# Kernel optimization log

Measured on AMD Instinct MI355X. Metric: run time of the kernel, lower is better.

## Reference

```python
import jax, jax.numpy as jnp
import numpy as np

B, T, C = 2, 2048, 1024
E = 8            # num_experts
K = 2            # num_active (top-k)
H = 4 * C        # expert hidden dim


def setup_inputs() -> dict:
    key = jax.random.key(0)
    ks = jax.random.split(key, 8)
    s = 0.02
    return {
        "x": jax.random.normal(ks[0], (B, T, C), dtype=jnp.float32),
        "Wg": jax.random.normal(ks[1], (C, E), dtype=jnp.float32) * s,
        "bg": jnp.zeros((E,), dtype=jnp.float32),
        "W1": jax.random.normal(ks[2], (E, C, H), dtype=jnp.float32) * s,
        "b1": jnp.zeros((E, H), dtype=jnp.float32),
        "W2": jax.random.normal(ks[3], (E, H, C), dtype=jnp.float32) * s,
        "b2": jnp.zeros((E, C), dtype=jnp.float32),
    }


def reference(x, Wg, bg, W1, b1, W2, b2):
    Bs, Ts, Cs = x.shape
    x_flat = x.reshape(-1, Cs)                       # [N, C]
    gate_logits = x_flat @ Wg + bg                   # [N, E]
    gates = jax.nn.softmax(gate_logits, axis=-1)
    w, idx = jax.lax.top_k(gates, K)                 # [N, K]
    w = w / jnp.sum(w, axis=-1, keepdims=True)
    # combine[n, e] = sum_k w[n,k] * (idx[n,k] == e); zero for unrouted experts,
    # so weighting the dense per-expert output reproduces the masked scatter-add.
    combine = jnp.sum(jax.nn.one_hot(idx, E, dtype=x.dtype) * w[..., None], axis=1)  # [N, E]
    out = jnp.zeros_like(x_flat)
    for e in range(E):  # small fixed expert loop; GEMM-dominated
        h = jax.nn.gelu(x_flat @ W1[e] + b1[e], approximate=False)  # [N, H]
        y = h @ W2[e] + b2[e]                                       # [N, C]
        out = out + y * combine[:, e:e + 1]
    return out.reshape(Bs, Ts, Cs)
```

## Files before the change

kernel.cpp:

```cpp
#include <hip/hip_runtime.h>
#include <hip/hip_bf16.h>
#include <math.h>

#define NTOK  4096
#define CDIM  1024
#define HDIM  4096
#define NEXP  8
#define TOPK  2

using short8 = __attribute__((ext_vector_type(8))) short;
using f32x4  = __attribute__((ext_vector_type(4))) float;

__device__ inline ushort f2bf(float f) {
    uint32_t u = __builtin_bit_cast(uint32_t, f);
    uint32_t r = (u + 0x7FFFu + ((u >> 16) & 1u)) >> 16;
    return (ushort)r;
}

__device__ __forceinline__ void gl_lds16(const void* g, void* l) {
    __builtin_amdgcn_global_load_lds(
        (const __attribute__((address_space(1))) void*)(void*)g,
        (__attribute__((address_space(3))) void*)l, 16, 0, 0);
}

__global__ __launch_bounds__(256)
void gate_kernel(const float* __restrict__ x, const float* __restrict__ Wg,
                 const float* __restrict__ bg, int* __restrict__ counts,
                 int* __restrict__ tlist, float* __restrict__ wslot,
                 ushort* __restrict__ xbf) {
    int wave = threadIdx.x >> 6, lane = threadIdx.x & 63;
    int t = blockIdx.x * 4 + wave;
    const float* xr = x + (size_t)t * CDIM;

    float acc[NEXP];
#pragma unroll
    for (int e = 0; e < NEXP; e++) acc[e] = 0.f;

#pragma unroll
    for (int i = 0; i < CDIM / 64; i++) {
        int c = lane + 64 * i;
        float xv = xr[c];
        xbf[(size_t)t * CDIM + c] = f2bf(xv);
        const float* wr = Wg + (size_t)c * NEXP;
#pragma unroll
        for (int e = 0; e < NEXP; e++) acc[e] += xv * wr[e];
    }
#pragma unroll
    for (int e = 0; e < NEXP; e++) {
        float v = acc[e];
        for (int off = 32; off > 0; off >>= 1) v += __shfl_xor(v, off);
        acc[e] = v + bg[e];
    }
    if (lane == 0) {
        int i1 = 0; float m1 = acc[0];
#pragma unroll
        for (int e = 1; e < NEXP; e++) if (acc[e] > m1) { m1 = acc[e]; i1 = e; }
        int i2 = -1; float m2 = -1e30f;
#pragma unroll
        for (int e = 0; e < NEXP; e++) if (e != i1 && acc[e] > m2) { m2 = acc[e]; i2 = e; }
        float w0 = 1.f / (1.f + expf(m2 - m1));
        float w1 = 1.f - w0;
        int p0 = atomicAdd(&counts[i1], 1);
        tlist[i1 * NTOK + p0] = t * 2;
        int p1 = atomicAdd(&counts[i2], 1);
        tlist[i2 * NTOK + p1] = t * 2 + 1;
        wslot[t * 2]     = w0;
        wslot[t * 2 + 1] = w1;
    }
}

__global__ __launch_bounds__(256)
void transpose_kernel(const float* __restrict__ in, ushort* __restrict__ out,
                      int R, int Ccols) {
    __shared__ ushort tile[64 * 64];
    int e = blockIdx.z;
    const float* src = in + (size_t)e * R * Ccols;
    ushort* dst = out + (size_t)e * Ccols * R;
    int c0 = blockIdx.x * 64, r0 = blockIdx.y * 64;
    int tid = threadIdx.x;
    int tx = tid & 15, ty = tid >> 4;

    float4 v[4];
#pragma unroll
    for (int j = 0; j < 4; j++)
        v[j] = *(const float4*)&src[(size_t)(r0 + ty * 4 + j) * Ccols + c0 + tx * 4];

#pragma unroll
    for (int i = 0; i < 4; i++) {
        int c = tx * 4 + i;
        uint2 pr;
        pr.x = (uint)f2bf(v[0][i]) | ((uint)f2bf(v[1][i]) << 16);
        pr.y = (uint)f2bf(v[2][i]) | ((uint)f2bf(v[3][i]) << 16);
        int gr = (ty >> 1) ^ ((c >> 2) & 7);
        int off = c * 128 + (gr << 4) + (ty & 1) * 8;
        *(uint2*)((char*)tile + off) = pr;
    }
    __syncthreads();

#pragma unroll
    for (int p = 0; p < 2; p++) {
        int c   = (tid >> 3) + 32 * p;
        int rch = tid & 7;
        int gr  = rch ^ ((c >> 2) & 7);
        short8 val = *(short8*)((char*)tile + c * 128 + (gr << 4));
        *(short8*)&dst[(size_t)(c0 + c) * R + r0 + rch * 8] = val;
    }
}

template<int GELU, int OUTBF16>
__global__ __launch_bounds__(256, 3)
void moe_gemm(const ushort* __restrict__ A, const ushort* __restrict__ Bt,
              const float* __restrict__ bias, const int* __restrict__ tlist,
              const int* __restrict__ counts, void* __restrict__ Out,
              int K, int N, int ashift, int nxmask, int nxshift, int ksplit,
              size_t psz) {
    int flat = blockIdx.x;
    int e  = flat & 7;
    int j  = flat >> 3;
    int mt = j & 31;
    int nj = j >> 5;
    int cnt = counts[e];
    int m0 = mt * 128;
    if (m0 >= cnt) return;
    int n0 = (nj & nxmask) * 128;
    int split = nj >> nxshift;
    int kbeg = split * ksplit;

    __shared__ ushort As[2][128 * 32];
    __shared__ ushort Bs[2][128 * 32];
    __shared__ int rowv[128];

    int tid = threadIdx.x;
    if (tid < 128) {
        int r = m0 + tid;
        rowv[tid] = tlist[e * NTOK + (r < cnt ? r : cnt - 1)];
    }
    __syncthreads();

    const ushort* Be = Bt + (size_t)e * N * K;

    int lane = tid & 63, w = tid >> 6;
    int wm = (w >> 1) * 64, wn = (w & 1) * 64;
    int quad = lane >> 4, l16 = lane & 15;

    int srow   = tid >> 2;
    int schunk = (tid & 3) ^ ((tid >> 3) & 3);
    const ushort* pa0 = A  + (size_t)(rowv[srow]      >> ashift) * K + kbeg + schunk * 8;
    const ushort* pa1 = A  + (size_t)(rowv[srow + 64] >> ashift) * K + kbeg + schunk * 8;
    const ushort* pb0 = Be + (size_t)(n0 + srow)      * K + kbeg + schunk * 8;
    const ushort* pb1 = Be + (size_t)(n0 + srow + 64) * K + kbeg + schunk * 8;

    int swr  = quad ^ ((l16 >> 1) & 3);
    int aidx = (wm + l16) * 32 + swr * 8;
    int bidx = (wn + l16) * 32 + swr * 8;

    f32x4 acc[4][4] = {};

    auto STAGE = [&](int buf) {
        gl_lds16(pa0, &As[buf][(w * 16) * 32]);
        gl_lds16(pa1, &As[buf][(w * 16 + 64) * 32]);
        gl_lds16(pb0, &Bs[buf][(w * 16) * 32]);
        gl_lds16(pb1, &Bs[buf][(w * 16 + 64) * 32]);
        pa0 += 32; pa1 += 32; pb0 += 32; pb1 += 32;
    };
    auto COMPUTE = [&](int buf) {
        short8 a[4], b[4];
#pragma unroll
        for (int mti = 0; mti < 4; mti++) a[mti] = *(short8*)&As[buf][aidx + mti * 512];
#pragma unroll
        for (int nti = 0; nti < 4; nti++) b[nti] = *(short8*)&Bs[buf][bidx + nti * 512];
#pragma unroll
        for (int mti = 0; mti < 4; mti++)
#pragma unroll
            for (int nti = 0; nti < 4; nti++)
                acc[mti][nti] = __builtin_amdgcn_mfma_f32_16x16x32_bf16(
                    a[mti], b[nti], acc[mti][nti], 0, 0, 0);
    };

    int nsteps = ksplit >> 5;
    STAGE(0);
    __syncthreads();
    for (int i = 0; i < nsteps - 2; i += 2) {
        STAGE(1);
        COMPUTE(0);
        __syncthreads();
        STAGE(0);
        COMPUTE(1);
        __syncthreads();
    }
    STAGE(1);
    COMPUTE(0);
    __syncthreads();
    COMPUTE(1);

    float* outF = (float*)Out + split * psz;
    ushort* outH = (ushort*)Out;
    const float* be = bias + (size_t)e * N;
#pragma unroll
    for (int mti = 0; mti < 4; mti++) {
#pragma unroll
        for (int r = 0; r < 4; r++) {
            int lrow = wm + mti * 16 + quad * 4 + r;
            if (m0 + lrow < cnt) {
                int v = rowv[lrow];
                size_t base = (size_t)v * N;
#pragma unroll
                for (int nti = 0; nti < 4; nti++) {
                    int col = n0 + wn + nti * 16 + l16;
                    float val = acc[mti][nti][r] + (split == 0 ? be[col] : 0.f);
                    if (GELU) val = 0.5f * val * (1.0f + erff(val * 0.70710678118654752f));
                    if (OUTBF16) outH[base + col] = f2bf(val);
                    else         outF[base + col] = val;
                }
            }
        }
    }
}

__global__ __launch_bounds__(256)
void combine_kernel(const float* __restrict__ y, const float* __restrict__ wslot,
                    float* __restrict__ out) {
    const float* y2 = y + (size_t)NTOK * TOPK * CDIM;
    int idx = blockIdx.x * 256 + threadIdx.x;
    int c4 = idx & (CDIM / 4 - 1);
    int t = idx >> 8;
    float w0 = wslot[2 * t], w1 = wslot[2 * t + 1];
    const float4* y0a = (const float4*)(y  + (size_t)(2 * t) * CDIM);
    const float4* y1a = (const float4*)(y  + (size_t)(2 * t + 1) * CDIM);
    const float4* y0b = (const float4*)(y2 + (size_t)(2 * t) * CDIM);
    const float4* y1b = (const float4*)(y2 + (size_t)(2 * t + 1) * CDIM);
    float4 a0 = y0a[c4], a1 = y0b[c4], b0 = y1a[c4], b1 = y1b[c4], o;
    o.x = w0 * (a0.x + a1.x) + w1 * (b0.x + b1.x);
    o.y = w0 * (a0.y + a1.y) + w1 * (b0.y + b1.y);
    o.z = w0 * (a0.z + a1.z) + w1 * (b0.z + b1.z);
    o.w = w0 * (a0.w + a1.w) + w1 * (b0.w + b1.w);
    ((float4*)(out + (size_t)t * CDIM))[c4] = o;
}

extern "C" void kernel_launch(void* const* d_in, const int* in_sizes, int n_in,
                              void* d_out, int out_size, void* d_ws, size_t ws_size,
                              hipStream_t stream) {
    const float* x  = (const float*)d_in[0];
    const float* Wg = (const float*)d_in[1];
    const float* bg = (const float*)d_in[2];
    const float* W1 = (const float*)d_in[3];
    const float* b1 = (const float*)d_in[4];
    const float* W2 = (const float*)d_in[5];
    const float* b2 = (const float*)d_in[6];
    float* out = (float*)d_out;
    char* ws = (char*)d_ws;

    size_t off = 0;
    int*    counts = (int*)(ws + off);    off += 256;
    int*    tlist  = (int*)(ws + off);    off += (size_t)NEXP * NTOK * 4;
    float*  wslot  = (float*)(ws + off);  off += (size_t)NTOK * TOPK * 4;
    ushort* xbf    = (ushort*)(ws + off); off += (size_t)NTOK * CDIM * 2;
    ushort* WT     = (ushort*)(ws + off); off += (size_t)NEXP * CDIM * HDIM * 2;
    ushort* h      = (ushort*)(ws + off); off += (size_t)NTOK * TOPK * HDIM * 2;
    float*  y      = (float*)(ws + off);  off += (size_t)NTOK * TOPK * CDIM * 4 * 2;

    hipMemsetAsync(counts, 0, NEXP * sizeof(int), stream);

    gate_kernel<<<NTOK / 4, 256, 0, stream>>>(x, Wg, bg, counts, tlist, wslot, xbf);

    transpose_kernel<<<dim3(HDIM / 64, CDIM / 64, NEXP), 256, 0, stream>>>(
        W1, WT, CDIM, HDIM);

    moe_gemm<1, 1><<<NEXP * 32 * (HDIM / 128), 256, 0, stream>>>(
        xbf, WT, b1, tlist, counts, (void*)h, CDIM, HDIM, 1,
        HDIM / 128 - 1, 5, CDIM, 0);

    transpose_kernel<<<dim3(CDIM / 64, HDIM / 64, NEXP), 256, 0, stream>>>(
        W2, WT, HDIM, CDIM);

    moe_gemm<0, 0><<<NEXP * 32 * (CDIM / 128) * 2, 256, 0, stream>>>(
        h, WT, b2, tlist, counts, (void*)y, HDIM, CDIM, 0,
        CDIM / 128 - 1, 3, HDIM / 2, (size_t)NTOK * TOPK * CDIM);

    combine_kernel<<<(NTOK * CDIM / 4) / 256, 256, 0, stream>>>(y, wslot, out);
}
```

Before: 687.4 us.

## Overlap next-tile loads with compute via explicit vmcnt waits and raw barriers

```diff
diff --git a/kernel.cpp b/kernel.cpp
--- a/kernel.cpp
+++ b/kernel.cpp
@@ -17,11 +17,23 @@
     return (ushort)r;
 }
 
+__device__ __forceinline__ float gelu_fast(float v) {
+    float z = fabsf(v) * 0.70710678118654752f;
+    float t = 1.0f / fmaf(0.3275911f, z, 1.0f);
+    float p = t * fmaf(t, fmaf(t, fmaf(t, fmaf(t, 1.061405429f, -1.453152027f),
+                                        1.421413741f), -0.284496736f), 0.254829592f);
+    float erfz = 1.0f - p * __expf(-z * z);
+    return 0.5f * v * (1.0f + copysignf(erfz, v));
+}
+
 __device__ __forceinline__ void gl_lds16(const void* g, void* l) {
     __builtin_amdgcn_global_load_lds(
         (const __attribute__((address_space(1))) void*)(void*)g,
         (__attribute__((address_space(3))) void*)l, 16, 0, 0);
 }
+
+#define SCHED_FENCE() __builtin_amdgcn_sched_barrier(0)
+#define RAW_BAR()  { SCHED_FENCE(); __builtin_amdgcn_s_barrier(); SCHED_FENCE(); }
 
 __global__ __launch_bounds__(256)
 void gate_kernel(const float* __restrict__ x, const float* __restrict__ Wg,
@@ -179,23 +191,25 @@
 
     int nsteps = ksplit >> 5;
     STAGE(0);
-    __syncthreads();
-    for (int i = 0; i < nsteps - 2; i += 2) {
-        STAGE(1);
-        COMPUTE(0);
-        __syncthreads();
-        STAGE(0);
-        COMPUTE(1);
-        __syncthreads();
-    }
-    STAGE(1);
-    COMPUTE(0);
-    __syncthreads();
-    COMPUTE(1);
+    for (int i = 0; i < nsteps - 1; ++i) {
+        int b = i & 1;
+        STAGE(1 - b);
+        asm volatile("s_waitcnt vmcnt(4)" ::: "memory");
+        RAW_BAR();
+        COMPUTE(b);
+        RAW_BAR();
+    }
+    asm volatile("s_waitcnt vmcnt(0)" ::: "memory");
+    RAW_BAR();
+    COMPUTE((nsteps - 1) & 1);
 
     float* outF = (float*)Out + split * psz;
     ushort* outH = (ushort*)Out;
     const float* be = bias + (size_t)e * N;
+    float bv[4];
+#pragma unroll
+    for (int nti = 0; nti < 4; nti++)
+        bv[nti] = (split == 0) ? be[n0 + wn + nti * 16 + l16] : 0.f;
 #pragma unroll
     for (int mti = 0; mti < 4; mti++) {
 #pragma unroll
@@ -207,8 +221,8 @@
 #pragma unroll
                 for (int nti = 0; nti < 4; nti++) {
                     int col = n0 + wn + nti * 16 + l16;
-                    float val = acc[mti][nti][r] + (split == 0 ? be[col] : 0.f);
-                    if (GELU) val = 0.5f * val * (1.0f + erff(val * 0.70710678118654752f));
+                    float val = acc[mti][nti][r] + bv[nti];
+                    if (GELU) val = gelu_fast(val);
                     if (OUTBF16) outH[base + col] = f2bf(val);
                     else         outF[base + col] = val;
                 }
```

Result: faster. 656.8 us (-4.4%).
